# Kernel tuning notes

Measured on AMD Instinct MI355X. Metric: run time of the kernel, lower is better.

Reference implementation:

```python
import jax, jax.numpy as jnp
import numpy as np

TOP_K_PERCENT = 0.7


def setup_inputs() -> dict:
    key = jax.random.key(0)
    k1, k2, k3, k4 = jax.random.split(key, 4)
    B, C, H, W = 4, 19, 512, 1024
    logits = jax.random.normal(k1, (B, C, H, W), dtype=jnp.float32)
    labels = jax.random.randint(k2, (B, H, W), 0, C, dtype=jnp.int64)
    smooth_labels = jax.random.uniform(k3, (B, C, H, W), dtype=jnp.float32)
    weight2 = jax.random.uniform(k4, (C,), dtype=jnp.float32)
    return {"logits": logits, "labels": labels, "smooth_labels": smooth_labels, "weight2": weight2}


def reference(logits, labels, smooth_labels, weight2):
    # Fused equivalent of the per-class loop:
    #   cum[b,h,w] = sum_c smooth[b,c,h,w] * weight2[c] * (-log_softmax(logits)[b,c,h,w])
    # (ignore_label=-1 never matches any class index, so no masking occurs.)
    logp = jax.nn.log_softmax(logits, axis=1)  # [B,C,H,W]
    w = weight2[None, :, None, None]
    pixel_losses_2 = -(smooth_labels * w * logp).sum(axis=1)  # [B,H,W]
    flat = pixel_losses_2.reshape(-1)
    k = int(TOP_K_PERCENT * flat.shape[0])  # static shape -> python int
    top_vals, _ = jax.lax.top_k(flat, k)
    return top_vals.mean()
```

## Files before the change

### kernel.cpp

```cpp
#include <hip/hip_runtime.h>

#define NPIX     2097152
#define NT4      524288
#define NCH      19
#define KSEL     1468006u
#define NBLK     2048
#define H1B      4096
#define H23B     1024
#define NHB      128

#define OFF_ROWS  (NPIX*4)
#define OFF_COMB1 (OFF_ROWS + NHB*H1B*4)
#define OFF_COMB2 (OFF_COMB1 + H1B*4)
#define OFF_PART  (OFF_COMB2 + H23B*4)
#define OFF_CTRL  (OFF_PART + NBLK*8)

struct Ctrl { unsigned p1, n1, p2, n2, T, r2; };

__global__ __launch_bounds__(256) void k_loss(
    const float* __restrict__ logits, const float* __restrict__ smooth,
    const float* __restrict__ wgt, float* __restrict__ loss)
{
    int tid = blockIdx.x * 256 + threadIdx.x;
    int img = tid >> 17;
    int rem = tid & 131071;
    const float4* L = (const float4*)logits + (size_t)img * (NCH * 131072) + rem;
    const float4* S = (const float4*)smooth + (size_t)img * (NCH * 131072) + rem;

    float4 xb[4], sb[4];
    #pragma unroll
    for (int i = 0; i < 4; ++i) {
        xb[i] = L[(size_t)i * 131072];
        sb[i] = S[(size_t)i * 131072];
    }

    float m0 = -3.4e38f, m1 = -3.4e38f, m2 = -3.4e38f, m3 = -3.4e38f;
    float s0 = 0.f, s1 = 0.f, s2 = 0.f, s3 = 0.f;
    float sw0 = 0.f, sw1 = 0.f, sw2 = 0.f, sw3 = 0.f;
    float swl0 = 0.f, swl1 = 0.f, swl2 = 0.f, swl3 = 0.f;

    #pragma unroll
    for (int c = 0; c < NCH; ++c) {
        float4 xv = xb[c & 3];
        float4 sv = sb[c & 3];
        if (c + 4 < NCH) {
            xb[c & 3] = L[(size_t)(c + 4) * 131072];
            sb[c & 3] = S[(size_t)(c + 4) * 131072];
        }
        float wc = wgt[c];

        float n0 = fmaxf(m0, xv.x), n1 = fmaxf(m1, xv.y);
        float n2 = fmaxf(m2, xv.z), n3 = fmaxf(m3, xv.w);
        s0 = s0 * __expf(m0 - n0) + __expf(xv.x - n0);
        s1 = s1 * __expf(m1 - n1) + __expf(xv.y - n1);
        s2 = s2 * __expf(m2 - n2) + __expf(xv.z - n2);
        s3 = s3 * __expf(m3 - n3) + __expf(xv.w - n3);
        m0 = n0; m1 = n1; m2 = n2; m3 = n3;

        float t0 = sv.x * wc, t1 = sv.y * wc, t2 = sv.z * wc, t3 = sv.w * wc;
        sw0 += t0; sw1 += t1; sw2 += t2; sw3 += t3;
        swl0 += t0 * xv.x; swl1 += t1 * xv.y;
        swl2 += t2 * xv.z; swl3 += t3 * xv.w;
    }

    float l0 = fmaxf((m0 + __logf(s0)) * sw0 - swl0, 0.f);
    float l1 = fmaxf((m1 + __logf(s1)) * sw1 - swl1, 0.f);
    float l2 = fmaxf((m2 + __logf(s2)) * sw2 - swl2, 0.f);
    float l3 = fmaxf((m3 + __logf(s3)) * sw3 - swl3, 0.f);

    ((float4*)loss)[tid] = make_float4(l0, l1, l2, l3);
}

__global__ __launch_bounds__(256) void k_hist1(
    const uint4* __restrict__ lossbits, unsigned* __restrict__ rows)
{
    __shared__ unsigned h[H1B];
    int t = threadIdx.x;
    #pragma unroll
    for (int j = t; j < H1B; j += 256) h[j] = 0;
    __syncthreads();
    int base = blockIdx.x * (NT4 / NHB);
    for (int i = t; i < NT4 / NHB; i += 256) {
        uint4 v = lossbits[base + i];
        atomicAdd(&h[v.x >> 20], 1u);
        atomicAdd(&h[v.y >> 20], 1u);
        atomicAdd(&h[v.z >> 20], 1u);
        atomicAdd(&h[v.w >> 20], 1u);
    }
    __syncthreads();
    for (int j = t; j < H1B; j += 256)
        rows[blockIdx.x * H1B + j] = h[j];
}

__global__ __launch_bounds__(256) void k_histr(
    const uint4* __restrict__ lossbits, const Ctrl* __restrict__ ctrl,
    unsigned* __restrict__ rows, int lvl)
{
    __shared__ unsigned h[H23B];
    unsigned pref = (lvl == 0) ? ctrl->p1 : ctrl->p2;
    int ms = (lvl == 0) ? 20 : 10;
    int bs = (lvl == 0) ? 10 : 0;
    int t = threadIdx.x;
    #pragma unroll
    for (int j = t; j < H23B; j += 256) h[j] = 0;
    __syncthreads();
    int base = blockIdx.x * (NT4 / NHB);
    for (int i = t; i < NT4 / NHB; i += 256) {
        uint4 v = lossbits[base + i];
        if ((v.x >> ms) == pref) atomicAdd(&h[(v.x >> bs) & 1023u], 1u);
        if ((v.y >> ms) == pref) atomicAdd(&h[(v.y >> bs) & 1023u], 1u);
        if ((v.z >> ms) == pref) atomicAdd(&h[(v.z >> bs) & 1023u], 1u);
        if ((v.w >> ms) == pref) atomicAdd(&h[(v.w >> bs) & 1023u], 1u);
    }
    __syncthreads();
    for (int j = t; j < H23B; j += 256)
        rows[blockIdx.x * H23B + j] = h[j];
}

__global__ __launch_bounds__(256) void k_reduce(
    const unsigned* __restrict__ rows, unsigned* __restrict__ comb, int nbins)
{
    int i = blockIdx.x * 256 + threadIdx.x;
    unsigned s = 0;
    for (int b = 0; b < NHB; ++b) s += rows[b * nbins + i];
    comb[i] = s;
}

__global__ __launch_bounds__(256) void k_sel1(
    const unsigned* __restrict__ comb, Ctrl* __restrict__ ctrl)
{
    __shared__ unsigned bins[H1B];
    __shared__ unsigned cs[256];
    __shared__ unsigned sh_t0, sh_base;
    int t = threadIdx.x;
    for (int j = t; j < H1B; j += 256) bins[j] = comb[j];
    __syncthreads();
    unsigned sum = 0;
    #pragma unroll
    for (int j = 0; j < 16; ++j) sum += bins[t * 16 + j];
    cs[t] = sum; __syncthreads();
    for (int off = 1; off < 256; off <<= 1) {
        unsigned v = (t + off < 256) ? cs[t + off] : 0u;
        __syncthreads();
        cs[t] += v;
        __syncthreads();
    }
    unsigned St = cs[t], Sn = (t < 255) ? cs[t + 1] : 0u;
    if (St >= KSEL && Sn < KSEL) { sh_t0 = (unsigned)t; sh_base = Sn; }
    __syncthreads();
    if (t == 0) {
        unsigned cum = sh_base;
        for (int b = (int)sh_t0 * 16 + 15;; --b) {
            unsigned c = bins[b];
            if (cum + c >= KSEL) { ctrl->p1 = (unsigned)b; ctrl->n1 = KSEL - cum; break; }
            cum += c;
        }
    }
}

__global__ __launch_bounds__(256) void k_selr(
    const unsigned* __restrict__ comb, Ctrl* __restrict__ ctrl, int lvl)
{
    __shared__ unsigned bins[H23B];
    __shared__ unsigned cs[256];
    __shared__ unsigned sh_t0, sh_base;
    int t = threadIdx.x;
    unsigned need = (lvl == 0) ? ctrl->n1 : ctrl->n2;
    unsigned pref = (lvl == 0) ? ctrl->p1 : ctrl->p2;
    for (int j = t; j < H23B; j += 256) bins[j] = comb[j];
    __syncthreads();
    unsigned sum = bins[t*4] + bins[t*4+1] + bins[t*4+2] + bins[t*4+3];
    cs[t] = sum; __syncthreads();
    for (int off = 1; off < 256; off <<= 1) {
        unsigned v = (t + off < 256) ? cs[t + off] : 0u;
        __syncthreads();
        cs[t] += v;
        __syncthreads();
    }
    unsigned St = cs[t], Sn = (t < 255) ? cs[t + 1] : 0u;
    if (St >= need && Sn < need) { sh_t0 = (unsigned)t; sh_base = Sn; }
    __syncthreads();
    if (t == 0) {
        unsigned cum = sh_base;
        for (int b = (int)sh_t0 * 4 + 3;; --b) {
            unsigned c = bins[b];
            if (cum + c >= need) {
                if (lvl == 0) { ctrl->p2 = (pref << 10) | (unsigned)b; ctrl->n2 = need - cum; }
                else          { ctrl->T  = (pref << 10) | (unsigned)b; ctrl->r2 = need - cum; }
                break;
            }
            cum += c;
        }
    }
}

__global__ __launch_bounds__(256) void k_sum(
    const uint4* __restrict__ lossbits, const Ctrl* __restrict__ ctrl,
    double* __restrict__ partials)
{
    unsigned T = ctrl->T;
    int tid = blockIdx.x * 256 + threadIdx.x;
    uint4 v = lossbits[tid];
    double acc = 0.0;
    if (v.x > T) acc += (double)__uint_as_float(v.x);
    if (v.y > T) acc += (double)__uint_as_float(v.y);
    if (v.z > T) acc += (double)__uint_as_float(v.z);
    if (v.w > T) acc += (double)__uint_as_float(v.w);
    #pragma unroll
    for (int off = 32; off > 0; off >>= 1) acc += __shfl_down(acc, off, 64);
    __shared__ double wsum[4];
    int lane = threadIdx.x & 63, wid = threadIdx.x >> 6;
    if (lane == 0) wsum[wid] = acc;
    __syncthreads();
    if (threadIdx.x == 0)
        partials[blockIdx.x] = wsum[0] + wsum[1] + wsum[2] + wsum[3];
}

__global__ __launch_bounds__(256) void k_final(
    const double* __restrict__ partials, const Ctrl* __restrict__ ctrl,
    float* __restrict__ out)
{
    double acc = 0.0;
    for (int i = threadIdx.x; i < NBLK; i += 256) acc += partials[i];
    #pragma unroll
    for (int off = 32; off > 0; off >>= 1) acc += __shfl_down(acc, off, 64);
    __shared__ double wsum[4];
    int lane = threadIdx.x & 63, wid = threadIdx.x >> 6;
    if (lane == 0) wsum[wid] = acc;
    __syncthreads();
    if (threadIdx.x == 0) {
        double tot = wsum[0] + wsum[1] + wsum[2] + wsum[3];
        tot += (double)ctrl->r2 * (double)__uint_as_float(ctrl->T);
        out[0] = (float)(tot / (double)KSEL);
    }
}

extern "C" void kernel_launch(void* const* d_in, const int* in_sizes, int n_in,
                              void* d_out, int out_size, void* d_ws, size_t ws_size,
                              hipStream_t stream)
{
    const float* logits = (const float*)d_in[0];
    const float* smooth = (const float*)d_in[2];
    const float* wgt    = (const float*)d_in[3];

    char* ws = (char*)d_ws;
    float*    loss     = (float*)ws;
    unsigned* rows     = (unsigned*)(ws + OFF_ROWS);
    unsigned* comb1    = (unsigned*)(ws + OFF_COMB1);
    unsigned* comb2    = (unsigned*)(ws + OFF_COMB2);
    double*   partials = (double*)(ws + OFF_PART);
    Ctrl*     ctrl     = (Ctrl*)(ws + OFF_CTRL);
    const uint4* lb    = (const uint4*)loss;

    k_loss  <<<NBLK, 256, 0, stream>>>(logits, smooth, wgt, loss);
    k_hist1 <<<NHB, 256, 0, stream>>>(lb, rows);
    k_reduce<<<H1B / 256, 256, 0, stream>>>(rows, comb1, H1B);
    k_sel1  <<<1, 256, 0, stream>>>(comb1, ctrl);
    k_histr <<<NHB, 256, 0, stream>>>(lb, ctrl, rows, 0);
    k_reduce<<<H23B / 256, 256, 0, stream>>>(rows, comb2, H23B);
    k_selr  <<<1, 256, 0, stream>>>(comb2, ctrl, 0);
    k_histr <<<NHB, 256, 0, stream>>>(lb, ctrl, rows, 1);
    k_reduce<<<H23B / 256, 256, 0, stream>>>(rows, comb2, H23B);
    k_selr  <<<1, 256, 0, stream>>>(comb2, ctrl, 1);
    k_sum   <<<NBLK, 256, 0, stream>>>(lb, ctrl, partials);
    k_final <<<1, 256, 0, stream>>>(partials, ctrl, (float*)d_out);
}
```

Baseline: 375.3 us.

## Fuse radix-select histogram, reduce, select and sum stages into one cooperative kernel

Measured after the change: 522.8 us. +39.3%, slower.

```diff
diff --git a/kernel.cpp b/kernel.cpp
--- a/kernel.cpp
+++ b/kernel.cpp
@@ -1,27 +1,31 @@
 #include <hip/hip_runtime.h>
+#include <hip/hip_cooperative_groups.h>
+
+namespace cg = cooperative_groups;
 
 #define NPIX     2097152
 #define NT4      524288
 #define NCH      19
 #define KSEL     1468006u
-#define NBLK     2048
+#define K1_BLK   512
+#define K1_GRID  (NT4 / K1_BLK)
+#define SGRID    128
 #define H1B      4096
-#define H23B     1024
-#define NHB      128
+#define SLICE    (NT4 / SGRID)
 
 #define OFF_ROWS  (NPIX*4)
-#define OFF_COMB1 (OFF_ROWS + NHB*H1B*4)
+#define OFF_COMB1 (OFF_ROWS + SGRID*H1B*4)
 #define OFF_COMB2 (OFF_COMB1 + H1B*4)
-#define OFF_PART  (OFF_COMB2 + H23B*4)
-#define OFF_CTRL  (OFF_PART + NBLK*8)
+#define OFF_PART  (OFF_COMB2 + 1024*4)
+#define OFF_CTRL  (OFF_PART + SGRID*8)
 
 struct Ctrl { unsigned p1, n1, p2, n2, T, r2; };
 
-__global__ __launch_bounds__(256) void k_loss(
+__global__ __launch_bounds__(K1_BLK) void k_loss(
     const float* __restrict__ logits, const float* __restrict__ smooth,
     const float* __restrict__ wgt, float* __restrict__ loss)
 {
-    int tid = blockIdx.x * 256 + threadIdx.x;
+    int tid = blockIdx.x * K1_BLK + threadIdx.x;
     int img = tid >> 17;
     int rem = tid & 131071;
     const float4* L = (const float4*)logits + (size_t)img * (NCH * 131072) + rem;
@@ -71,16 +75,25 @@
     ((float4*)loss)[tid] = make_float4(l0, l1, l2, l3);
 }
 
-__global__ __launch_bounds__(256) void k_hist1(
-    const uint4* __restrict__ lossbits, unsigned* __restrict__ rows)
+__global__ __launch_bounds__(256) void k_select(
+    const uint4* __restrict__ lossbits, unsigned* __restrict__ rows,
+    unsigned* __restrict__ comb1, unsigned* __restrict__ comb2,
+    double* __restrict__ part, Ctrl* __restrict__ ctrl,
+    float* __restrict__ out)
 {
+    cg::grid_group grid = cg::this_grid();
     __shared__ unsigned h[H1B];
-    int t = threadIdx.x;
-    #pragma unroll
+    __shared__ unsigned cs[256];
+    __shared__ unsigned sh_t0, sh_base;
+    __shared__ double wsum[4];
+    const int t = threadIdx.x;
+    const int b = blockIdx.x;
+    const int base = b * SLICE;
+    volatile Ctrl* vc = (volatile Ctrl*)ctrl;
+
     for (int j = t; j < H1B; j += 256) h[j] = 0;
     __syncthreads();
-    int base = blockIdx.x * (NT4 / NHB);
-    for (int i = t; i < NT4 / NHB; i += 256) {
+    for (int i = t; i < SLICE; i += 256) {
         uint4 v = lossbits[base + i];
         atomicAdd(&h[v.x >> 20], 1u);
         atomicAdd(&h[v.y >> 20], 1u);
@@ -88,150 +101,134 @@
         atomicAdd(&h[v.w >> 20], 1u);
     }
     __syncthreads();
-    for (int j = t; j < H1B; j += 256)
-        rows[blockIdx.x * H1B + j] = h[j];
-}
-
-__global__ __launch_bounds__(256) void k_histr(
-    const uint4* __restrict__ lossbits, const Ctrl* __restrict__ ctrl,
-    unsigned* __restrict__ rows, int lvl)
-{
-    __shared__ unsigned h[H23B];
-    unsigned pref = (lvl == 0) ? ctrl->p1 : ctrl->p2;
-    int ms = (lvl == 0) ? 20 : 10;
-    int bs = (lvl == 0) ? 10 : 0;
-    int t = threadIdx.x;
-    #pragma unroll
-    for (int j = t; j < H23B; j += 256) h[j] = 0;
-    __syncthreads();
-    int base = blockIdx.x * (NT4 / NHB);
-    for (int i = t; i < NT4 / NHB; i += 256) {
-        uint4 v = lossbits[base + i];
-        if ((v.x >> ms) == pref) atomicAdd(&h[(v.x >> bs) & 1023u], 1u);
-        if ((v.y >> ms) == pref) atomicAdd(&h[(v.y >> bs) & 1023u], 1u);
-        if ((v.z >> ms) == pref) atomicAdd(&h[(v.z >> bs) & 1023u], 1u);
-        if ((v.w >> ms) == pref) atomicAdd(&h[(v.w >> bs) & 1023u], 1u);
-    }
-    __syncthreads();
-    for (int j = t; j < H23B; j += 256)
-        rows[blockIdx.x * H23B + j] = h[j];
-}
-
-__global__ __launch_bounds__(256) void k_reduce(
-    const unsigned* __restrict__ rows, unsigned* __restrict__ comb, int nbins)
-{
-    int i = blockIdx.x * 256 + threadIdx.x;
-    unsigned s = 0;
-    for (int b = 0; b < NHB; ++b) s += rows[b * nbins + i];
-    comb[i] = s;
-}
-
-__global__ __launch_bounds__(256) void k_sel1(
-    const unsigned* __restrict__ comb, Ctrl* __restrict__ ctrl)
-{
-    __shared__ unsigned bins[H1B];
-    __shared__ unsigned cs[256];
-    __shared__ unsigned sh_t0, sh_base;
-    int t = threadIdx.x;
-    for (int j = t; j < H1B; j += 256) bins[j] = comb[j];
-    __syncthreads();
-    unsigned sum = 0;
-    #pragma unroll
-    for (int j = 0; j < 16; ++j) sum += bins[t * 16 + j];
-    cs[t] = sum; __syncthreads();
-    for (int off = 1; off < 256; off <<= 1) {
-        unsigned v = (t + off < 256) ? cs[t + off] : 0u;
-        __syncthreads();
-        cs[t] += v;
-        __syncthreads();
-    }
-    unsigned St = cs[t], Sn = (t < 255) ? cs[t + 1] : 0u;
-    if (St >= KSEL && Sn < KSEL) { sh_t0 = (unsigned)t; sh_base = Sn; }
-    __syncthreads();
-    if (t == 0) {
-        unsigned cum = sh_base;
-        for (int b = (int)sh_t0 * 16 + 15;; --b) {
-            unsigned c = bins[b];
-            if (cum + c >= KSEL) { ctrl->p1 = (unsigned)b; ctrl->n1 = KSEL - cum; break; }
-            cum += c;
-        }
-    }
-}
-
-__global__ __launch_bounds__(256) void k_selr(
-    const unsigned* __restrict__ comb, Ctrl* __restrict__ ctrl, int lvl)
-{
-    __shared__ unsigned bins[H23B];
-    __shared__ unsigned cs[256];
-    __shared__ unsigned sh_t0, sh_base;
-    int t = threadIdx.x;
-    unsigned need = (lvl == 0) ? ctrl->n1 : ctrl->n2;
-    unsigned pref = (lvl == 0) ? ctrl->p1 : ctrl->p2;
-    for (int j = t; j < H23B; j += 256) bins[j] = comb[j];
-    __syncthreads();
-    unsigned sum = bins[t*4] + bins[t*4+1] + bins[t*4+2] + bins[t*4+3];
-    cs[t] = sum; __syncthreads();
-    for (int off = 1; off < 256; off <<= 1) {
-        unsigned v = (t + off < 256) ? cs[t + off] : 0u;
-        __syncthreads();
-        cs[t] += v;
-        __syncthreads();
-    }
-    unsigned St = cs[t], Sn = (t < 255) ? cs[t + 1] : 0u;
-    if (St >= need && Sn < need) { sh_t0 = (unsigned)t; sh_base = Sn; }
-    __syncthreads();
-    if (t == 0) {
-        unsigned cum = sh_base;
-        for (int b = (int)sh_t0 * 4 + 3;; --b) {
-            unsigned c = bins[b];
-            if (cum + c >= need) {
-                if (lvl == 0) { ctrl->p2 = (pref << 10) | (unsigned)b; ctrl->n2 = need - cum; }
-                else          { ctrl->T  = (pref << 10) | (unsigned)b; ctrl->r2 = need - cum; }
-                break;
+    for (int j = t; j < H1B; j += 256) rows[b * H1B + j] = h[j];
+    grid.sync();
+
+    if (b < 16) {
+        int i = b * 256 + t;
+        unsigned s = 0;
+        for (int r = 0; r < SGRID; ++r) s += rows[r * H1B + i];
+        comb1[i] = s;
+    }
+    grid.sync();
+
+    if (b == 0) {
+        for (int j = t; j < H1B; j += 256) h[j] = comb1[j];
+        __syncthreads();
+        unsigned sum = 0;
+        #pragma unroll
+        for (int j = 0; j < 16; ++j) sum += h[t * 16 + j];
+        cs[t] = sum; __syncthreads();
+        for (int off = 1; off < 256; off <<= 1) {
+            unsigned v = (t + off < 256) ? cs[t + off] : 0u;
+            __syncthreads();
+            cs[t] += v;
+            __syncthreads();
+        }
+        unsigned St = cs[t], Sn = (t < 255) ? cs[t + 1] : 0u;
+        if (St >= KSEL && Sn < KSEL) { sh_t0 = (unsigned)t; sh_base = Sn; }
+        __syncthreads();
+        if (t == 0) {
+            unsigned cum = sh_base;
+            for (int bin = (int)sh_t0 * 16 + 15;; --bin) {
+                unsigned c = h[bin];
+                if (cum + c >= KSEL) { ctrl->p1 = (unsigned)bin; ctrl->n1 = KSEL - cum; break; }
+                cum += c;
             }
-            cum += c;
-        }
-    }
-}
-
-__global__ __launch_bounds__(256) void k_sum(
-    const uint4* __restrict__ lossbits, const Ctrl* __restrict__ ctrl,
-    double* __restrict__ partials)
-{
-    unsigned T = ctrl->T;
-    int tid = blockIdx.x * 256 + threadIdx.x;
-    uint4 v = lossbits[tid];
-    double acc = 0.0;
-    if (v.x > T) acc += (double)__uint_as_float(v.x);
-    if (v.y > T) acc += (double)__uint_as_float(v.y);
-    if (v.z > T) acc += (double)__uint_as_float(v.z);
-    if (v.w > T) acc += (double)__uint_as_float(v.w);
-    #pragma unroll
-    for (int off = 32; off > 0; off >>= 1) acc += __shfl_down(acc, off, 64);
-    __shared__ double wsum[4];
-    int lane = threadIdx.x & 63, wid = threadIdx.x >> 6;
-    if (lane == 0) wsum[wid] = acc;
-    __syncthreads();
-    if (threadIdx.x == 0)
-        partials[blockIdx.x] = wsum[0] + wsum[1] + wsum[2] + wsum[3];
-}
-
-__global__ __launch_bounds__(256) void k_final(
-    const double* __restrict__ partials, const Ctrl* __restrict__ ctrl,
-    float* __restrict__ out)
-{
-    double acc = 0.0;
-    for (int i = threadIdx.x; i < NBLK; i += 256) acc += partials[i];
-    #pragma unroll
-    for (int off = 32; off > 0; off >>= 1) acc += __shfl_down(acc, off, 64);
-    __shared__ double wsum[4];
-    int lane = threadIdx.x & 63, wid = threadIdx.x >> 6;
-    if (lane == 0) wsum[wid] = acc;
-    __syncthreads();
-    if (threadIdx.x == 0) {
-        double tot = wsum[0] + wsum[1] + wsum[2] + wsum[3];
-        tot += (double)ctrl->r2 * (double)__uint_as_float(ctrl->T);
-        out[0] = (float)(tot / (double)KSEL);
+        }
+    }
+    grid.sync();
+
+    #pragma unroll 1
+    for (int lvl = 0; lvl < 2; ++lvl) {
+        unsigned pref = (lvl == 0) ? vc->p1 : vc->p2;
+        unsigned need = (lvl == 0) ? vc->n1 : vc->n2;
+        int ms = (lvl == 0) ? 20 : 10;
+        int bs = (lvl == 0) ? 10 : 0;
+
+        for (int j = t; j < 1024; j += 256) h[j] = 0;
+        __syncthreads();
+        for (int i = t; i < SLICE; i += 256) {
+            uint4 v = lossbits[base + i];
+            if ((v.x >> ms) == pref) atomicAdd(&h[(v.x >> bs) & 1023u], 1u);
+            if ((v.y >> ms) == pref) atomicAdd(&h[(v.y >> bs) & 1023u], 1u);
+            if ((v.z >> ms) == pref) atomicAdd(&h[(v.z >> bs) & 1023u], 1u);
+            if ((v.w >> ms) == pref) atomicAdd(&h[(v.w >> bs) & 1023u], 1u);
+        }
+        __syncthreads();
+        for (int j = t; j < 1024; j += 256) rows[b * 1024 + j] = h[j];
+        grid.sync();
+
+        if (b < 4) {
+            int i = b * 256 + t;
+            unsigned s = 0;
+            for (int r = 0; r < SGRID; ++r) s += rows[r * 1024 + i];
+            comb2[i] = s;
+        }
+        grid.sync();
+
+        if (b == 0) {
+            for (int j = t; j < 1024; j += 256) h[j] = comb2[j];
+            __syncthreads();
+            unsigned sum = h[t*4] + h[t*4+1] + h[t*4+2] + h[t*4+3];
+            cs[t] = sum; __syncthreads();
+            for (int off = 1; off < 256; off <<= 1) {
+                unsigned v = (t + off < 256) ? cs[t + off] : 0u;
+                __syncthreads();
+                cs[t] += v;
+                __syncthreads();
+            }
+            unsigned St = cs[t], Sn = (t < 255) ? cs[t + 1] : 0u;
+            if (St >= need && Sn < need) { sh_t0 = (unsigned)t; sh_base = Sn; }
+            __syncthreads();
+            if (t == 0) {
+                unsigned cum = sh_base;
+                for (int bin = (int)sh_t0 * 4 + 3;; --bin) {
+                    unsigned c = h[bin];
+                    if (cum + c >= need) {
+                        if (lvl == 0) { ctrl->p2 = (pref << 10) | (unsigned)bin; ctrl->n2 = need - cum; }
+                        else          { ctrl->T  = (pref << 10) | (unsigned)bin; ctrl->r2 = need - cum; }
+                        break;
+                    }
+                    cum += c;
+                }
+            }
+        }
+        grid.sync();
+    }
+
+    {
+        unsigned T = vc->T;
+        double acc = 0.0;
+        for (int i = t; i < SLICE; i += 256) {
+            uint4 v = lossbits[base + i];
+            if (v.x > T) acc += (double)__uint_as_float(v.x);
+            if (v.y > T) acc += (double)__uint_as_float(v.y);
+            if (v.z > T) acc += (double)__uint_as_float(v.z);
+            if (v.w > T) acc += (double)__uint_as_float(v.w);
+        }
+        #pragma unroll
+        for (int off = 32; off > 0; off >>= 1) acc += __shfl_down(acc, off, 64);
+        int lane = t & 63, wid = t >> 6;
+        if (lane == 0) wsum[wid] = acc;
+        __syncthreads();
+        if (t == 0) part[b] = wsum[0] + wsum[1] + wsum[2] + wsum[3];
+    }
+    grid.sync();
+
+    if (b == 0) {
+        double acc = (t < SGRID) ? part[t] : 0.0;
+        #pragma unroll
+        for (int off = 32; off > 0; off >>= 1) acc += __shfl_down(acc, off, 64);
+        int lane = t & 63, wid = t >> 6;
+        __syncthreads();
+        if (lane == 0) wsum[wid] = acc;
+        __syncthreads();
+        if (t == 0) {
+            double tot = wsum[0] + wsum[1] + wsum[2] + wsum[3];
+            tot += (double)vc->r2 * (double)__uint_as_float(vc->T);
+            out[0] = (float)(tot / (double)KSEL);
+        }
     }
 }
 
@@ -244,24 +241,19 @@
     const float* wgt    = (const float*)d_in[3];
 
     char* ws = (char*)d_ws;
-    float*    loss     = (float*)ws;
-    unsigned* rows     = (unsigned*)(ws + OFF_ROWS);
-    unsigned* comb1    = (unsigned*)(ws + OFF_COMB1);
-    unsigned* comb2    = (unsigned*)(ws + OFF_COMB2);
-    double*   partials = (double*)(ws + OFF_PART);
-    Ctrl*     ctrl     = (Ctrl*)(ws + OFF_CTRL);
-    const uint4* lb    = (const uint4*)loss;
-
-    k_loss  <<<NBLK, 256, 0, stream>>>(logits, smooth, wgt, loss);
-    k_hist1 <<<NHB, 256, 0, stream>>>(lb, rows);
-    k_reduce<<<H1B / 256, 256, 0, stream>>>(rows, comb1, H1B);
-    k_sel1  <<<1, 256, 0, stream>>>(comb1, ctrl);
-    k_histr <<<NHB, 256, 0, stream>>>(lb, ctrl, rows, 0);
-    k_reduce<<<H23B / 256, 256, 0, stream>>>(rows, comb2, H23B);
-    k_selr  <<<1, 256, 0, stream>>>(comb2, ctrl, 0);
-    k_histr <<<NHB, 256, 0, stream>>>(lb, ctrl, rows, 1);
-    k_reduce<<<H23B / 256, 256, 0, stream>>>(rows, comb2, H23B);
-    k_selr  <<<1, 256, 0, stream>>>(comb2, ctrl, 1);
-    k_sum   <<<NBLK, 256, 0, stream>>>(lb, ctrl, partials);
-    k_final <<<1, 256, 0, stream>>>(partials, ctrl, (float*)d_out);
+    float*    loss  = (float*)ws;
+    unsigned* rows  = (unsigned*)(ws + OFF_ROWS);
+    unsigned* comb1 = (unsigned*)(ws + OFF_COMB1);
+    unsigned* comb2 = (unsigned*)(ws + OFF_COMB2);
+    double*   part  = (double*)(ws + OFF_PART);
+    Ctrl*     ctrl  = (Ctrl*)(ws + OFF_CTRL);
+    const uint4* lb = (const uint4*)loss;
+    float* outp     = (float*)d_out;
+
+    k_loss<<<K1_GRID, K1_BLK, 0, stream>>>(logits, smooth, wgt, loss);
+
+    void* args[] = { (void*)&lb, (void*)&rows, (void*)&comb1, (void*)&comb2,
+                     (void*)&part, (void*)&ctrl, (void*)&outp };
+    hipLaunchCooperativeKernel((void*)k_select, dim3(SGRID), dim3(256),
+                               args, 0, stream);
 }
```
